# Performance work log

Hardware: AMD Instinct MI355X
Metric: run time of the kernel (lower is better)

## Reference

```python
import jax, jax.numpy as jnp
import numpy as np

# Config constants (from init_kwargs)
RADIUS_UPDATE_RATE = 0.01
MIN_RADIUS = 0.1
MAX_RADIUS = 2.0
EPS = 1e-6


def _finite(x, fallback):
    """nan/inf guard: replace non-finite entries with fallback (same math as torch.where(isnan|isinf,...))."""
    bad = jnp.isnan(x) | jnp.isinf(x)
    return jnp.where(bad, fallback, x)


def _compute_score(r, causal=True):
    """QuantumAttention.compute_score: relu'd 2-D dot-product interaction,
    causal mask, row-normalized. r: [B,S,2] -> score: [B,S,S]."""
    raw = jnp.einsum('bse,bte->bst', r, r)          # thin bmm, inner dim 2
    score = jax.nn.relu(raw)
    if causal:
        S = r.shape[1]
        mask = jnp.tril(jnp.ones((S, S), dtype=bool))
        score = jnp.where(mask[None, :, :], score, 0.0)
    denom = jnp.clip(jnp.sum(score, axis=-1, keepdims=True), EPS, None)
    return score / denom


def setup_inputs() -> dict:
    key = jax.random.key(0)
    k1, k2 = jax.random.split(key)
    B, S = 4, 4096
    r_embed = jax.random.normal(k1, (B, S, 2), dtype=jnp.float32)
    # dt in a realistic (dt_scale .. dt_max) range
    dt = jax.random.uniform(k2, (B,), dtype=jnp.float32, minval=1e-4, maxval=1e-2)
    return {"r_embed": r_embed, "dt": dt}


def reference(r_embed, dt):
    # Heun-Euler integration step with radius rescale.
    dt_e = dt[:, None, None]                         # [B,1,1]

    # Stage 1 (k1)
    score = _compute_score(r_embed, causal=True)     # [B,S,S]
    context = jnp.einsum('bst,bte->bse', score, r_embed)
    k1 = _finite(dt_e * context, 0.0)
    r_mid = _finite(r_embed + k1, r_embed)

    # Stage 2 (k2)
    score_mid = _compute_score(r_mid, causal=True)
    context_mid = jnp.einsum('bst,bte->bse', score_mid, r_mid)
    k2 = _finite(dt_e * context_mid, 0.0)

    # Final update + radius adjustment
    r_new = r_embed + 0.5 * (k1 + k2)
    new_radius = jnp.clip(jnp.linalg.norm(r_new, axis=-1, keepdims=True), EPS, None)
    radius_adjustment = jnp.sum(score, axis=-1, keepdims=True) * RADIUS_UPDATE_RATE
    adjusted_radius = jnp.clip(new_radius + radius_adjustment, MIN_RADIUS, MAX_RADIUS)
    scale_factor = adjusted_radius / new_radius
    r_final = r_new * scale_factor
    r_final = _finite(r_final, r_embed)
    return r_final, score
```

## Files before the change

kernel.cpp:

```cpp
#include <hip/hip_runtime.h>
#include <math.h>


#define S_LEN 4096
#define ROWS  16384
#define BLK   256
#define EPSF  1e-6f
#define RATE  0.01f
#define MINR  0.1f
#define MAXR  2.0f


__global__ __launch_bounds__(BLK) void k_prep(
    const float2* __restrict__ r_in,
    const float*  __restrict__ dt_in,
    float* __restrict__ ws)
{
    const int lane = threadIdx.x & 63;
    const int row  = (blockIdx.x << 2) + (threadIdx.x >> 6);
    const int b = row >> 12;
    const int s = row & (S_LEN - 1);
    const float2* rb  = r_in + ((size_t)b << 12);
    const float4* rb4 = (const float4*)rb;
    const float2 rs = rb[s];

    float dsum = 0.f, nx = 0.f, ny = 0.f;
    for (int i = lane; 2*i <= s; i += 64) {
        float4 p = rb4[i];
        float d0 = fmaxf(rs.x * p.x + rs.y * p.y, 0.f);
        dsum += d0; nx = fmaf(d0, p.x, nx); ny = fmaf(d0, p.y, ny);
        if (2*i + 1 <= s) {
            float d1 = fmaxf(rs.x * p.z + rs.y * p.w, 0.f);
            dsum += d1; nx = fmaf(d1, p.z, nx); ny = fmaf(d1, p.w, ny);
        }
    }
    #pragma unroll
    for (int off = 32; off > 0; off >>= 1) {
        dsum += __shfl_down(dsum, off);
        nx   += __shfl_down(nx, off);
        ny   += __shfl_down(ny, off);
    }

    if (lane == 0) {
        const float D   = dsum;
        const float dc  = fmaxf(D, EPSF);
        const float dtb = dt_in[b];
        float k1x = dtb * nx / dc;
        float k1y = dtb * ny / dc;
        if (!isfinite(k1x)) k1x = 0.f;
        if (!isfinite(k1y)) k1y = 0.f;
        float rmx = rs.x + k1x, rmy = rs.y + k1y;
        if (!isfinite(rmx)) rmx = rs.x;
        if (!isfinite(rmy)) rmy = rs.y;
        ws[2*row]              = rmx;  ws[2*row + 1]          = rmy;
        ws[2*ROWS + 2*row]     = k1x;  ws[2*ROWS + 2*row + 1] = k1y;
        ws[4*ROWS + row]       = D / dc;
        ws[5*ROWS + row]       = 1.f / dc;
    }
}

__global__ __launch_bounds__(BLK) void k_main(
    const float2* __restrict__ r_in,
    const float*  __restrict__ dt_in,
    const float*  __restrict__ ws,
    float* __restrict__ score_out,
    float* __restrict__ rfinal_out)
{
    __shared__ float4 lds4[2048];

    const int lane = threadIdx.x & 63;
    const int row  = (blockIdx.x << 2) + (threadIdx.x >> 6);
    const int b = row >> 12;
    const int s = row & (S_LEN - 1);
    const float4* rb4 = (const float4*)(r_in + ((size_t)b << 12));

    #pragma unroll
    for (int k = 0; k < 8; k++)
        lds4[threadIdx.x + (k << 8)] = rb4[threadIdx.x + (k << 8)];

    const float2 rs  = ((const float2*)r_in)[((size_t)b << 12) + s];
    const float  inv = ws[5*ROWS + row];
    __syncthreads();

    const float isx = rs.x * inv, isy = rs.y * inv;
    float* orow = score_out + (size_t)row * S_LEN;
    #pragma unroll 4
    for (int q = 0; q < 16; q++) {
        const int t0 = (lane << 2) + (q << 8);
        float4 v = make_float4(0.f, 0.f, 0.f, 0.f);
        if ((q << 8) <= s) {
            if (t0 <= s) {
                const float4 p01 = lds4[t0 >> 1];
                const float4 p23 = lds4[(t0 >> 1) + 1];
                v.x = fmaxf(isx * p01.x + isy * p01.y, 0.f);
                v.y = (t0 + 1 <= s) ? fmaxf(isx * p01.z + isy * p01.w, 0.f) : 0.f;
                v.z = (t0 + 2 <= s) ? fmaxf(isx * p23.x + isy * p23.y, 0.f) : 0.f;
                v.w = (t0 + 3 <= s) ? fmaxf(isx * p23.z + isy * p23.w, 0.f) : 0.f;
            }
        }
        *((float4*)(orow + t0)) = v;
    }

    const float4* rm4 = (const float4*)((const float2*)ws + ((size_t)b << 12));
    const float2  ms  = ((const float2*)ws)[((size_t)b << 12) + s];

    float dsum = 0.f, nx = 0.f, ny = 0.f;
    for (int i = lane; 2*i <= s; i += 64) {
        float4 p = rm4[i];
        float d0 = fmaxf(ms.x * p.x + ms.y * p.y, 0.f);
        dsum += d0; nx = fmaf(d0, p.x, nx); ny = fmaf(d0, p.y, ny);
        if (2*i + 1 <= s) {
            float d1 = fmaxf(ms.x * p.z + ms.y * p.w, 0.f);
            dsum += d1; nx = fmaf(d1, p.z, nx); ny = fmaf(d1, p.w, ny);
        }
    }
    #pragma unroll
    for (int off = 32; off > 0; off >>= 1) {
        dsum += __shfl_down(dsum, off);
        nx   += __shfl_down(nx, off);
        ny   += __shfl_down(ny, off);
    }

    if (lane == 0) {
        const float dc  = fmaxf(dsum, EPSF);
        const float dtb = dt_in[b];
        float k2x = dtb * nx / dc;
        float k2y = dtb * ny / dc;
        if (!isfinite(k2x)) k2x = 0.f;
        if (!isfinite(k2y)) k2y = 0.f;
        const float2 r0  = r_in[row];
        const float  k1x = ws[2*ROWS + 2*row], k1y = ws[2*ROWS + 2*row + 1];
        const float rnx = r0.x + 0.5f * (k1x + k2x);
        const float rny = r0.y + 0.5f * (k1y + k2y);
        const float nr  = fmaxf(sqrtf(rnx*rnx + rny*rny), EPSF);
        const float ar  = fminf(fmaxf(nr + ws[4*ROWS + row] * RATE, MINR), MAXR);
        const float sc  = ar / nr;
        float fx = rnx * sc, fy = rny * sc;
        if (!isfinite(fx)) fx = r0.x;
        if (!isfinite(fy)) fy = r0.y;
        rfinal_out[2*row]     = fx;
        rfinal_out[2*row + 1] = fy;
    }
}

extern "C" void kernel_launch(void* const* d_in, const int* in_sizes, int n_in,
                              void* d_out, int out_size, void* d_ws, size_t ws_size,
                              hipStream_t stream) {
    const float2* r_in  = (const float2*)d_in[0];
    const float*  dt_in = (const float*)d_in[1];
    float* out = (float*)d_out;
    float* ws  = (float*)d_ws;

    float* rfinal_out = out;
    float* score_out  = out + (size_t)2 * ROWS;

    hipLaunchKernelGGL(k_prep, dim3(ROWS / 4), dim3(BLK), 0, stream,
                       r_in, dt_in, ws);
    hipLaunchKernelGGL(k_main, dim3(ROWS / 4), dim3(BLK), 0, stream,
                       r_in, dt_in, ws, score_out, rfinal_out);
}
```

Baseline: 276.2 us.

## Split score writing into 2D tiled blocks separate from final-update blocks

```diff
diff --git a/kernel.cpp b/kernel.cpp
--- a/kernel.cpp
+++ b/kernel.cpp
@@ -9,6 +9,11 @@
 #define RATE  0.01f
 #define MINR  0.1f
 #define MAXR  2.0f
+
+#define CB 16
+#define GB 8
+#define SCORE_BLOCKS (4*CB*GB)
+#define FIN_BLOCKS   (ROWS/4)
 
 
 __global__ __launch_bounds__(BLK) void k_prep(
@@ -66,80 +71,100 @@
     float* __restrict__ score_out,
     float* __restrict__ rfinal_out)
 {
-    __shared__ float4 lds4[2048];
+    __shared__ float2 lds_r[512];
+    __shared__ float  lds_inv[512];
 
+    const int wave = threadIdx.x >> 6;
     const int lane = threadIdx.x & 63;
-    const int row  = (blockIdx.x << 2) + (threadIdx.x >> 6);
-    const int b = row >> 12;
-    const int s = row & (S_LEN - 1);
-    const float4* rb4 = (const float4*)(r_in + ((size_t)b << 12));
 
-    #pragma unroll
-    for (int k = 0; k < 8; k++)
-        lds4[threadIdx.x + (k << 8)] = rb4[threadIdx.x + (k << 8)];
+    if (blockIdx.x < SCORE_BLOCKS) {
+        const int sb   = blockIdx.x;
+        const int b    = sb >> 7;
+        const int rem  = sb & 127;
+        const int c    = rem >> 3;
+        const int g    = rem & 7;
+        const int col0 = c << 8;
+        const int rbase= g << 9;
 
-    const float2 rs  = ((const float2*)r_in)[((size_t)b << 12) + s];
-    const float  inv = ws[5*ROWS + row];
-    __syncthreads();
+        const float4* rb4 = (const float4*)(r_in + ((size_t)b << 12));
 
-    const float isx = rs.x * inv, isy = rs.y * inv;
-    float* orow = score_out + (size_t)row * S_LEN;
-    #pragma unroll 4
-    for (int q = 0; q < 16; q++) {
-        const int t0 = (lane << 2) + (q << 8);
-        float4 v = make_float4(0.f, 0.f, 0.f, 0.f);
-        if ((q << 8) <= s) {
-            if (t0 <= s) {
-                const float4 p01 = lds4[t0 >> 1];
-                const float4 p23 = lds4[(t0 >> 1) + 1];
-                v.x = fmaxf(isx * p01.x + isy * p01.y, 0.f);
-                v.y = (t0 + 1 <= s) ? fmaxf(isx * p01.z + isy * p01.w, 0.f) : 0.f;
-                v.z = (t0 + 2 <= s) ? fmaxf(isx * p23.x + isy * p23.y, 0.f) : 0.f;
-                v.w = (t0 + 3 <= s) ? fmaxf(isx * p23.z + isy * p23.w, 0.f) : 0.f;
+        ((float4*)lds_r)[threadIdx.x] = rb4[(rbase >> 1) + threadIdx.x];
+        ((float2*)lds_inv)[threadIdx.x] =
+            ((const float2*)(ws + 5*(size_t)ROWS + ((size_t)b << 12) + rbase))[threadIdx.x];
+
+        const float4 p01 = rb4[(col0 >> 1) + 2*lane];
+        const float4 p23 = rb4[(col0 >> 1) + 2*lane + 1];
+        __syncthreads();
+
+        const int   t0g  = col0 + (lane << 2);
+        const int   lr0  = wave << 7;
+        float* base = score_out
+            + (size_t)(((size_t)b << 12) + rbase + lr0) * S_LEN + t0g;
+
+        #pragma unroll 4
+        for (int i = 0; i < 128; ++i) {
+            const int lr = lr0 + i;
+            const int r  = rbase + lr;
+            float4 v = make_float4(0.f, 0.f, 0.f, 0.f);
+            if (r >= col0) {
+                const float2 rs  = lds_r[lr];
+                const float  inv = lds_inv[lr];
+                const float isx = rs.x * inv, isy = rs.y * inv;
+                const float a0 = fmaxf(isx * p01.x + isy * p01.y, 0.f);
+                const float a1 = fmaxf(isx * p01.z + isy * p01.w, 0.f);
+                const float a2 = fmaxf(isx * p23.x + isy * p23.y, 0.f);
+                const float a3 = fmaxf(isx * p23.z + isy * p23.w, 0.f);
+                v.x = (t0g     <= r) ? a0 : 0.f;
+                v.y = (t0g + 1 <= r) ? a1 : 0.f;
+                v.z = (t0g + 2 <= r) ? a2 : 0.f;
+                v.w = (t0g + 3 <= r) ? a3 : 0.f;
+            }
+            *((float4*)(base + (size_t)i * S_LEN)) = v;
+        }
+    } else {
+        const int row = ((blockIdx.x - SCORE_BLOCKS) << 2) + wave;
+        const int b = row >> 12;
+        const int s = row & (S_LEN - 1);
+        const float4* rm4 = (const float4*)((const float2*)ws + ((size_t)b << 12));
+        const float2  ms  = ((const float2*)ws)[((size_t)b << 12) + s];
+
+        float dsum = 0.f, nx = 0.f, ny = 0.f;
+        for (int i = lane; 2*i <= s; i += 64) {
+            float4 p = rm4[i];
+            float d0 = fmaxf(ms.x * p.x + ms.y * p.y, 0.f);
+            dsum += d0; nx = fmaf(d0, p.x, nx); ny = fmaf(d0, p.y, ny);
+            if (2*i + 1 <= s) {
+                float d1 = fmaxf(ms.x * p.z + ms.y * p.w, 0.f);
+                dsum += d1; nx = fmaf(d1, p.z, nx); ny = fmaf(d1, p.w, ny);
             }
         }
-        *((float4*)(orow + t0)) = v;
-    }
+        #pragma unroll
+        for (int off = 32; off > 0; off >>= 1) {
+            dsum += __shfl_down(dsum, off);
+            nx   += __shfl_down(nx, off);
+            ny   += __shfl_down(ny, off);
+        }
 
-    const float4* rm4 = (const float4*)((const float2*)ws + ((size_t)b << 12));
-    const float2  ms  = ((const float2*)ws)[((size_t)b << 12) + s];
-
-    float dsum = 0.f, nx = 0.f, ny = 0.f;
-    for (int i = lane; 2*i <= s; i += 64) {
-        float4 p = rm4[i];
-        float d0 = fmaxf(ms.x * p.x + ms.y * p.y, 0.f);
-        dsum += d0; nx = fmaf(d0, p.x, nx); ny = fmaf(d0, p.y, ny);
-        if (2*i + 1 <= s) {
-            float d1 = fmaxf(ms.x * p.z + ms.y * p.w, 0.f);
-            dsum += d1; nx = fmaf(d1, p.z, nx); ny = fmaf(d1, p.w, ny);
+        if (lane == 0) {
+            const float dc  = fmaxf(dsum, EPSF);
+            const float dtb = dt_in[b];
+            float k2x = dtb * nx / dc;
+            float k2y = dtb * ny / dc;
+            if (!isfinite(k2x)) k2x = 0.f;
+            if (!isfinite(k2y)) k2y = 0.f;
+            const float2 r0  = r_in[row];
+            const float  k1x = ws[2*(size_t)ROWS + 2*row], k1y = ws[2*(size_t)ROWS + 2*row + 1];
+            const float rnx = r0.x + 0.5f * (k1x + k2x);
+            const float rny = r0.y + 0.5f * (k1y + k2y);
+            const float nr  = fmaxf(sqrtf(rnx*rnx + rny*rny), EPSF);
+            const float ar  = fminf(fmaxf(nr + ws[4*(size_t)ROWS + row] * RATE, MINR), MAXR);
+            const float sc  = ar / nr;
+            float fx = rnx * sc, fy = rny * sc;
+            if (!isfinite(fx)) fx = r0.x;
+            if (!isfinite(fy)) fy = r0.y;
+            rfinal_out[2*row]     = fx;
+            rfinal_out[2*row + 1] = fy;
         }
-    }
-    #pragma unroll
-    for (int off = 32; off > 0; off >>= 1) {
-        dsum += __shfl_down(dsum, off);
-        nx   += __shfl_down(nx, off);
-        ny   += __shfl_down(ny, off);
-    }
-
-    if (lane == 0) {
-        const float dc  = fmaxf(dsum, EPSF);
-        const float dtb = dt_in[b];
-        float k2x = dtb * nx / dc;
-        float k2y = dtb * ny / dc;
-        if (!isfinite(k2x)) k2x = 0.f;
-        if (!isfinite(k2y)) k2y = 0.f;
-        const float2 r0  = r_in[row];
-        const float  k1x = ws[2*ROWS + 2*row], k1y = ws[2*ROWS + 2*row + 1];
-        const float rnx = r0.x + 0.5f * (k1x + k2x);
-        const float rny = r0.y + 0.5f * (k1y + k2y);
-        const float nr  = fmaxf(sqrtf(rnx*rnx + rny*rny), EPSF);
-        const float ar  = fminf(fmaxf(nr + ws[4*ROWS + row] * RATE, MINR), MAXR);
-        const float sc  = ar / nr;
-        float fx = rnx * sc, fy = rny * sc;
-        if (!isfinite(fx)) fx = r0.x;
-        if (!isfinite(fy)) fy = r0.y;
-        rfinal_out[2*row]     = fx;
-        rfinal_out[2*row + 1] = fy;
     }
 }
 
@@ -156,6 +181,6 @@
 
     hipLaunchKernelGGL(k_prep, dim3(ROWS / 4), dim3(BLK), 0, stream,
                        r_in, dt_in, ws);
-    hipLaunchKernelGGL(k_main, dim3(ROWS / 4), dim3(BLK), 0, stream,
+    hipLaunchKernelGGL(k_main, dim3(SCORE_BLOCKS + FIN_BLOCKS), dim3(BLK), 0, stream,
                        r_in, dt_in, ws, score_out, rfinal_out);
 }
```

Measured after the change: 283.9 us. 1.03x slower.
